# Optimization experiments

Hardware: AMD Instinct MI355X
Metric: run time of the kernel (lower is better)

Reference implementation:

```python
import jax, jax.numpy as jnp
import numpy as np

DT = 0.05
DELAY = int(1.0 / DT)  # 20 steps of synaptic delay
NUM_ASCS = 2
R_MEM = 0.1     # membrane resistance
SIGMA_V = 1.0   # sigmoid smoothing of spiking nonlinearity
V_RESET = 0.0

B, T, IN, HID, OUT = 64, 200, 512, 1024, 512


def setup_inputs() -> dict:
    key = jax.random.key(0)
    ks = jax.random.split(key, 10)
    return {
        "x": jax.random.normal(ks[0], (B, T, IN), dtype=jnp.float32),
        "W_in": jax.random.normal(ks[1], (IN, HID), dtype=jnp.float32) / np.sqrt(IN),
        "W_lat": jax.random.normal(ks[2], (HID, HID), dtype=jnp.float32) / np.sqrt(HID),
        "thresh": jax.random.normal(ks[3], (1, HID), dtype=jnp.float32) * 0.1,
        "trans_k_m": jax.random.normal(ks[4], (1, HID), dtype=jnp.float32) * 0.1,
        "trans_asc_k": jax.random.normal(ks[5], (NUM_ASCS, 1, HID), dtype=jnp.float32) * 0.1,
        "asc_amp": jax.random.normal(ks[6], (NUM_ASCS, 1, HID), dtype=jnp.float32) * 0.1,
        "trans_asc_r": jax.random.normal(ks[7], (NUM_ASCS, 1, HID), dtype=jnp.float32) * 0.1,
        "W_out": jax.random.normal(ks[8], (OUT, HID), dtype=jnp.float32) / np.sqrt(HID),
        "b_out": jax.random.normal(ks[9], (OUT,), dtype=jnp.float32) * 0.01,
    }


def _glifr_rnn(x, W_in, W_lat, thresh, trans_k_m, trans_asc_k, asc_amp, trans_asc_r, W_out, b_out):
    Bx, Tx, _ = x.shape
    H = W_lat.shape[0]
    # rate transforms keep dt*k in (0,1); r in (-1,1)
    k_m = jax.nn.sigmoid(trans_k_m) / DT          # [1,H]
    k_asc = jax.nn.sigmoid(trans_asc_k) / DT      # [A,1,H]
    asc_r = 1.0 - 2.0 * jax.nn.sigmoid(trans_asc_r)
    # precompute input projection for all timesteps: [T,B,H]
    x_proj = jnp.swapaxes(jnp.einsum("bti,ih->bth", x, W_in), 0, 1)

    def step(carry, xp):
        firing, voltage, asc, buf = carry
        firing_delayed = buf[0]                       # firing DELAY steps ago
        syn = xp + firing_delayed @ W_lat             # synaptic current [B,H]
        asc_new = (asc_amp + asc_r * asc) * firing * (DT * k_asc) + (1.0 - DT * k_asc) * asc
        volt_new = (R_MEM * DT * k_m) * (syn + asc_new.sum(0)) \
                   + (1.0 - DT * k_m) * voltage + DT * k_m * V_RESET
        firing_new = jax.nn.sigmoid((volt_new - thresh) / SIGMA_V)
        buf_new = jnp.concatenate([buf[1:], firing_new[None]], axis=0)
        out = firing_new @ W_out.T + b_out            # per-step linear readout
        return (firing_new, volt_new, asc_new, buf_new), out

    z = jnp.zeros((Bx, H), dtype=x.dtype)
    carry0 = (z, z, jnp.zeros((NUM_ASCS, Bx, H), x.dtype), jnp.zeros((DELAY, Bx, H), x.dtype))
    _, outs = jax.lax.scan(step, carry0, x_proj)      # outs: [T,B,OUT]
    return jnp.swapaxes(outs, 0, 1)                   # [B,T,OUT]


def reference(x, W_in, W_lat, thresh, trans_k_m, trans_asc_k, asc_amp, trans_asc_r, W_out, b_out):
    return _glifr_rnn(x, W_in, W_lat, thresh, trans_k_m, trans_asc_k, asc_amp, trans_asc_r, W_out, b_out)
```

## Files before the change

kernel.cpp:

```cpp
#include <hip/hip_runtime.h>


typedef float f32x4 __attribute__((ext_vector_type(4)));
typedef __bf16 bf16x8 __attribute__((ext_vector_type(8)));
typedef unsigned short ushortx8 __attribute__((ext_vector_type(8)));
typedef unsigned short ushortx4 __attribute__((ext_vector_type(4)));

__device__ __forceinline__ unsigned short f2b(float f) {
    unsigned int u = __float_as_uint(f);
    unsigned int r = u + 0x7FFFu + ((u >> 16) & 1u);
    return (unsigned short)(r >> 16);
}
__device__ __forceinline__ float b2f(unsigned short u) {
    return __uint_as_float(((unsigned int)u) << 16);
}
__device__ __forceinline__ float sigmoidf(float x) {
    return 1.0f / (1.0f + __expf(-x));
}

__device__ __forceinline__ void gl_lds16(const unsigned short* g, unsigned short* l) {
    __builtin_amdgcn_global_load_lds(
        (const __attribute__((address_space(1))) void*)g,
        (__attribute__((address_space(3))) void*)l, 16, 0, 0);
}

__global__ __launch_bounds__(256) void prep_all(
    const float* __restrict__ W_in, const float* __restrict__ W_lat,
    const float* __restrict__ W_out, const float* __restrict__ x,
    unsigned short* __restrict__ WinT, unsigned short* __restrict__ WlatT,
    unsigned short* __restrict__ WoutB, unsigned short* __restrict__ xb)
{
    __shared__ unsigned short t[64][65];
    const int blk = blockIdx.x, tid = threadIdx.x;

    if (blk < 128) {
        int bx = (blk & 15) * 64, by = (blk >> 4) * 64;
        int tx = tid & 63, ty = tid >> 6;
        for (int r = ty; r < 64; r += 4)
            t[r][tx] = f2b(W_in[(size_t)(by + r) * 1024 + bx + tx]);
        __syncthreads();
        for (int r = ty; r < 64; r += 4)
            WinT[(size_t)(bx + r) * 512 + by + tx] = t[tx][r];
    } else if (blk < 384) {
        int b2 = blk - 128;
        int bx = (b2 & 15) * 64, by = (b2 >> 4) * 64;
        int tx = tid & 63, ty = tid >> 6;
        for (int r = ty; r < 64; r += 4)
            t[r][tx] = f2b(W_lat[(size_t)(by + r) * 1024 + bx + tx]);
        __syncthreads();
        for (int r = ty; r < 64; r += 4)
            WlatT[(size_t)(bx + r) * 1024 + by + tx] = t[tx][r];
    } else if (blk < 896) {
        int i = ((blk - 384) * 256 + tid) * 4;
        f32x4 v = *(const f32x4*)(W_out + i);
        ushortx4 o;
        o[0] = f2b(v[0]); o[1] = f2b(v[1]); o[2] = f2b(v[2]); o[3] = f2b(v[3]);
        *(ushortx4*)(WoutB + i) = o;
    } else {
        size_t i8 = (size_t)((blk - 896) * 256 + tid) * 8;
        int m = (int)(i8 >> 9), k = (int)(i8 & 511);
        int b = m & 63, tt = m >> 6;
        const float* src = x + ((size_t)b * 200 + tt) * 512 + k;
        f32x4 v0 = *(const f32x4*)src;
        f32x4 v1 = *(const f32x4*)(src + 4);
        ushortx8 o;
        o[0] = f2b(v0[0]); o[1] = f2b(v0[1]); o[2] = f2b(v0[2]); o[3] = f2b(v0[3]);
        o[4] = f2b(v1[0]); o[5] = f2b(v1[1]); o[6] = f2b(v1[2]); o[7] = f2b(v1[3]);
        *(ushortx8*)(xb + i8) = o;
    }
}

template<int BM, int BN, int MODE>
__global__ __launch_bounds__(256) void gemm_nt(
    const unsigned short* __restrict__ A,
    const unsigned short* __restrict__ Bt,
    float* __restrict__ outf,
    unsigned short* __restrict__ outb,
    const float* __restrict__ bias,
    int M, int N, int K, int t_base)
{
    constexpr int WM = BM / 2, WN = BN / 2;
    constexpr int TM = WM / 16, TN = WN / 16;

    __shared__ unsigned short Asm[BM * 64];
    __shared__ unsigned short Bsm[BN * 64];

    const int tid  = threadIdx.x;
    const int wave = tid >> 6, lane = tid & 63;
    const int m16  = lane & 15, quad = lane >> 4;
    const int nwg = gridDim.x * gridDim.y;
    const int d   = blockIdx.y * gridDim.x + blockIdx.x;
    const int l   = (d & 7) * (nwg >> 3) + (d >> 3);
    const int bm0 = (l / gridDim.x) * BM, bn0 = (l % gridDim.x) * BN;
    const int wr   = (wave >> 1) * WM, wc = (wave & 1) * WN;
    const int sr   = lane >> 3;
    const int sc   = lane & 7;

    f32x4 acc[TM][TN];
#pragma unroll
    for (int i = 0; i < TM; i++)
#pragma unroll
        for (int j = 0; j < TN; j++)
            acc[i][j] = (f32x4){0.f, 0.f, 0.f, 0.f};

    for (int k0 = 0; k0 < K; k0 += 64) {
#pragma unroll
        for (int g = wave; g < BM / 8; g += 4) {
            int r = g * 8 + sr;
            int c = sc ^ (r & 7);
            gl_lds16(A + (size_t)(bm0 + r) * K + k0 + c * 8, Asm + g * 512);
        }
#pragma unroll
        for (int g = wave; g < BN / 8; g += 4) {
            int r = g * 8 + sr;
            int c = sc ^ (r & 7);
            gl_lds16(Bt + (size_t)(bn0 + r) * K + k0 + c * 8, Bsm + g * 512);
        }
        __syncthreads();

        ushortx8 af[2][TM], bfr[2][TN];
#pragma unroll
        for (int kh = 0; kh < 2; kh++) {
#pragma unroll
            for (int i = 0; i < TM; i++) {
                int ra = wr + i * 16 + m16;
                af[kh][i] = *(const ushortx8*)(
                    Asm + ra * 64 + (((kh * 4 + quad) ^ (ra & 7)) * 8));
            }
#pragma unroll
            for (int j = 0; j < TN; j++) {
                int rb = wc + j * 16 + m16;
                bfr[kh][j] = *(const ushortx8*)(
                    Bsm + rb * 64 + (((kh * 4 + quad) ^ (rb & 7)) * 8));
            }
        }
#pragma unroll
        for (int i = 0; i < TM; i++)
#pragma unroll
            for (int j = 0; j < TN; j++) {
                acc[i][j] = __builtin_amdgcn_mfma_f32_16x16x32_bf16(
                    __builtin_bit_cast(bf16x8, af[0][i]),
                    __builtin_bit_cast(bf16x8, bfr[0][j]),
                    acc[i][j], 0, 0, 0);
                acc[i][j] = __builtin_amdgcn_mfma_f32_16x16x32_bf16(
                    __builtin_bit_cast(bf16x8, af[1][i]),
                    __builtin_bit_cast(bf16x8, bfr[1][j]),
                    acc[i][j], 0, 0, 0);
            }
        __syncthreads();
    }

#pragma unroll
    for (int i = 0; i < TM; i++)
#pragma unroll
        for (int j = 0; j < TN; j++) {
            int col = bn0 + wc + j * 16 + m16;
            float bv = (MODE == 2) ? bias[col] : 0.f;
#pragma unroll
            for (int v = 0; v < 4; v++) {
                int row = bm0 + wr + i * 16 + quad * 4 + v;
                if (MODE == 2) {
                    size_t o = (size_t)((row & 63) * 200 + t_base + (row >> 6)) * N + col;
                    outf[o] = acc[i][j][v] + bv;
                } else {
                    outb[(size_t)row * N + col] = f2b(acc[i][j][v]);
                }
            }
        }
}

__global__ __launch_bounds__(256) void fused_chunk(
    const unsigned short* __restrict__ Fprev,
    const unsigned short* __restrict__ Wlat,
    const unsigned short* __restrict__ xproj,
    float* __restrict__ state,
    unsigned short* __restrict__ Fc,
    const float* __restrict__ thresh,
    const float* __restrict__ t_km,
    const float* __restrict__ t_ak,
    const float* __restrict__ amp,
    const float* __restrict__ t_ar,
    int first)
{
    const int BH = 64 * 1024;
    __shared__ __align__(16) char lds[147456];
    unsigned short* A0 = (unsigned short*)lds;
    unsigned short* A1 = (unsigned short*)(lds + 40960);
    unsigned short* B0 = (unsigned short*)(lds + 81920);
    unsigned short* B1 = (unsigned short*)(lds + 114688);
    float* synT = (float*)lds;

    const int tid  = threadIdx.x;
    const int wave = tid >> 6, lane = tid & 63;
    const int m16  = lane & 15, quad = lane >> 4;
    const int sr2  = lane >> 5;
    const int sc32 = lane & 31;
    const int d    = blockIdx.y * 16 + blockIdx.x;
    const int l    = (d & 7) * 32 + (d >> 3);
    const int b0   = (l >> 4) * 4, h0 = (l & 15) * 64;
    const int wrow = (wave >> 1) * 48;
    const int wc   = (wave & 1) * 32;

    const int h    = h0 + lane;
    const int gidx = (b0 + wave) * 1024 + h;
    float th  = thresh[h];
    float sm  = sigmoidf(t_km[h]);
    float rm  = 0.1f * sm;
    float om  = 1.0f - sm;
    float sa0 = sigmoidf(t_ak[h]);
    float sa1 = sigmoidf(t_ak[1024 + h]);
    float am0 = amp[h];
    float am1 = amp[1024 + h];
    float r0  = 1.0f - 2.0f * sigmoidf(t_ar[h]);
    float r1  = 1.0f - 2.0f * sigmoidf(t_ar[1024 + h]);

    if (first) {
        float volt = 0.f, as0 = 0.f, as1 = 0.f, fir = 0.f;
#pragma unroll
        for (int s = 0; s < 20; s++) {
            float sv  = b2f(xproj[(size_t)(s * 64 + b0 + wave) * 1024 + h]);
            float na0 = (am0 + r0 * as0) * fir * sa0 + (1.f - sa0) * as0;
            float na1 = (am1 + r1 * as1) * fir * sa1 + (1.f - sa1) * as1;
            volt = rm * (sv + na0 + na1) + om * volt;
            fir  = sigmoidf(volt - th);
            Fc[(size_t)s * BH + gidx] = f2b(fir);
            as0 = na0; as1 = na1;
        }
        state[gidx]          = volt;
        state[BH + gidx]     = as0;
        state[2 * BH + gidx] = as1;
        state[3 * BH + gidx] = fir;
        return;
    }

    f32x4 acc[3][2];
#pragma unroll
    for (int i = 0; i < 3; i++) {
        if (i < 2 || wave < 2) {
#pragma unroll
            for (int j = 0; j < 2; j++)
#pragma unroll
                for (int v = 0; v < 4; v++) {
                    int row = wrow + i * 16 + quad * 4 + v;
                    int col = h0 + wc + j * 16 + m16;
                    acc[i][j][v] = b2f(
                        xproj[(size_t)(((row >> 2) << 6) + b0 + (row & 3)) * 1024 + col]);
                }
        }
    }

    auto STAGE = [&](unsigned short* Ad, unsigned short* Bd, int k0) {
        for (int g = wave; g < 40; g += 4) {
            int r = g * 2 + sr2;
            int c = sc32 ^ (r & 31);
            int m = ((r >> 2) << 6) + b0 + (r & 3);
            gl_lds16(Fprev + (size_t)m * 1024 + k0 + c * 8, Ad + g * 512);
        }
        for (int g = wave; g < 32; g += 4) {
            int r = g * 2 + sr2;
            int c = sc32 ^ (r & 31);
            gl_lds16(Wlat + (size_t)(h0 + r) * 1024 + k0 + c * 8, Bd + g * 512);
        }
    };
    auto COMPUTE = [&](const unsigned short* As, const unsigned short* Bs) {
#pragma unroll
        for (int half = 0; half < 2; half++) {
            ushortx8 af[4][3], bfr[4][2];
#pragma unroll
            for (int kh = 0; kh < 4; kh++) {
                int s = half * 16 + kh * 4 + quad;
#pragma unroll
                for (int i = 0; i < 3; i++) {
                    if (i < 2 || wave < 2) {
                        int ra = wrow + i * 16 + m16;
                        af[kh][i] = *(const ushortx8*)(
                            As + ra * 256 + ((s ^ (ra & 31)) * 8));
                    }
                }
#pragma unroll
                for (int j = 0; j < 2; j++) {
                    int rb = wc + j * 16 + m16;
                    bfr[kh][j] = *(const ushortx8*)(
                        Bs + rb * 256 + ((s ^ (rb & 31)) * 8));
                }
            }
#pragma unroll
            for (int i = 0; i < 3; i++) {
                if (i < 2 || wave < 2) {
#pragma unroll
                    for (int j = 0; j < 2; j++) {
#pragma unroll
                        for (int kh = 0; kh < 4; kh++) {
                            acc[i][j] = __builtin_amdgcn_mfma_f32_16x16x32_bf16(
                                __builtin_bit_cast(bf16x8, af[kh][i]),
                                __builtin_bit_cast(bf16x8, bfr[kh][j]), acc[i][j], 0, 0, 0);
                        }
                    }
                }
            }
        }
    };

    STAGE(A0, B0, 0);
    __syncthreads();
    STAGE(A1, B1, 256);  COMPUTE(A0, B0);  __syncthreads();
    STAGE(A0, B0, 512);  COMPUTE(A1, B1);  __syncthreads();
    STAGE(A1, B1, 768);  COMPUTE(A0, B0);  __syncthreads();
                         COMPUTE(A1, B1);  __syncthreads();

#pragma unroll
    for (int i = 0; i < 3; i++) {
        if (i < 2 || wave < 2) {
#pragma unroll
            for (int j = 0; j < 2; j++)
#pragma unroll
                for (int v = 0; v < 4; v++) {
                    int row = wrow + i * 16 + quad * 4 + v;
                    synT[row * 66 + wc + j * 16 + m16] = acc[i][j][v];
                }
        }
    }
    __syncthreads();

    float volt = state[gidx];
    float as0  = state[BH + gidx];
    float as1  = state[2 * BH + gidx];
    float fir  = state[3 * BH + gidx];

#pragma unroll
    for (int s = 0; s < 20; s++) {
        float sv  = synT[(s * 4 + wave) * 66 + lane];
        float na0 = (am0 + r0 * as0) * fir * sa0 + (1.f - sa0) * as0;
        float na1 = (am1 + r1 * as1) * fir * sa1 + (1.f - sa1) * as1;
        volt = rm * (sv + na0 + na1) + om * volt;
        fir  = sigmoidf(volt - th);
        Fc[(size_t)s * BH + gidx] = f2b(fir);
        as0 = na0; as1 = na1;
    }
    state[gidx]          = volt;
    state[BH + gidx]     = as0;
    state[2 * BH + gidx] = as1;
    state[3 * BH + gidx] = fir;
}

extern "C" void kernel_launch(void* const* d_in, const int* in_sizes, int n_in,
                              void* d_out, int out_size, void* d_ws, size_t ws_size,
                              hipStream_t stream)
{
    const float* x      = (const float*)d_in[0];
    const float* W_in   = (const float*)d_in[1];
    const float* W_lat  = (const float*)d_in[2];
    const float* thresh = (const float*)d_in[3];
    const float* t_km   = (const float*)d_in[4];
    const float* t_ak   = (const float*)d_in[5];
    const float* amp    = (const float*)d_in[6];
    const float* t_ar   = (const float*)d_in[7];
    const float* W_out  = (const float*)d_in[8];
    const float* b_out  = (const float*)d_in[9];
    float* out = (float*)d_out;

    char* ws = (char*)d_ws;
    unsigned short* synb  = (unsigned short*)ws;
    float*          state = (float*)(ws + 52428800);
    unsigned short* F     = (unsigned short*)(ws + 53477376);
    unsigned short* xb    = F;
    unsigned short* WinT  = (unsigned short*)(ws + 79691776);
    unsigned short* WlatT = (unsigned short*)(ws + 80740352);
    unsigned short* WoutB = (unsigned short*)(ws + 82837504);

    prep_all<<<4096, 256, 0, stream>>>(W_in, W_lat, W_out, x,
                                       WinT, WlatT, WoutB, xb);

    gemm_nt<128, 128, 0><<<dim3(1024 / 128, 12800 / 128), 256, 0, stream>>>(
        xb, WinT, nullptr, synb, nullptr, 12800, 1024, 512, 0);

    const size_t CHUNK = 20 * 64 * 1024;
    fused_chunk<<<dim3(16, 16), 256, 0, stream>>>(
        F, WlatT, synb, state, F, thresh, t_km, t_ak, amp, t_ar, 1);
    for (int c = 1; c < 10; c++) {
        fused_chunk<<<dim3(16, 16), 256, 0, stream>>>(
            F + (size_t)(c - 1) * CHUNK, WlatT,
            synb + (size_t)c * CHUNK, state, F + (size_t)c * CHUNK,
            thresh, t_km, t_ak, amp, t_ar, 0);
    }

    gemm_nt<128, 128, 2><<<dim3(512 / 128, 12800 / 128), 256, 0, stream>>>(
        F, WoutB, out, nullptr, b_out, 12800, 512, 1024, 0);
}
```

Baseline: 242.5 us.

## Split fused chunk kernel over 512 blocks with smaller batch tiles and K-steps

Each fused_chunk block now covers 2 batch rows instead of 4, so the grid grows from 256 to 512 blocks to fill more compute units. The K loop is restaged in 128-wide steps with 16-way swizzle, which shrinks LDS from 144KB to 56KB and could let more than one block share a CU. Each wave now computes a 40x16 output tile with three MFMA row tiles, the last one partly wasted. Only 128 of 256 threads run the serial recurrence, and W_lat is re-read by twice as many blocks.

```diff
diff --git a/kernel.cpp b/kernel.cpp
--- a/kernel.cpp
+++ b/kernel.cpp
@@ -183,42 +183,153 @@
     int first)
 {
     const int BH = 64 * 1024;
-    __shared__ __align__(16) char lds[147456];
+    __shared__ __align__(16) char lds[57344];
     unsigned short* A0 = (unsigned short*)lds;
-    unsigned short* A1 = (unsigned short*)(lds + 40960);
-    unsigned short* B0 = (unsigned short*)(lds + 81920);
-    unsigned short* B1 = (unsigned short*)(lds + 114688);
+    unsigned short* A1 = (unsigned short*)(lds + 12288);
+    unsigned short* B0 = (unsigned short*)(lds + 24576);
+    unsigned short* B1 = (unsigned short*)(lds + 40960);
     float* synT = (float*)lds;
 
     const int tid  = threadIdx.x;
     const int wave = tid >> 6, lane = tid & 63;
     const int m16  = lane & 15, quad = lane >> 4;
-    const int sr2  = lane >> 5;
-    const int sc32 = lane & 31;
+    const int sr4  = lane >> 4;
+    const int sc16 = lane & 15;
     const int d    = blockIdx.y * 16 + blockIdx.x;
-    const int l    = (d & 7) * 32 + (d >> 3);
-    const int b0   = (l >> 4) * 4, h0 = (l & 15) * 64;
-    const int wrow = (wave >> 1) * 48;
-    const int wc   = (wave & 1) * 32;
-
-    const int h    = h0 + lane;
-    const int gidx = (b0 + wave) * 1024 + h;
-    float th  = thresh[h];
-    float sm  = sigmoidf(t_km[h]);
-    float rm  = 0.1f * sm;
-    float om  = 1.0f - sm;
-    float sa0 = sigmoidf(t_ak[h]);
-    float sa1 = sigmoidf(t_ak[1024 + h]);
-    float am0 = amp[h];
-    float am1 = amp[1024 + h];
-    float r0  = 1.0f - 2.0f * sigmoidf(t_ar[h]);
-    float r1  = 1.0f - 2.0f * sigmoidf(t_ar[1024 + h]);
+    const int l    = (d & 7) * 64 + (d >> 3);
+    const int bg   = l >> 4;
+    const int h0   = (l & 15) * 64, b0 = bg * 2;
+    const int wc   = wave * 16;
 
     if (first) {
-        float volt = 0.f, as0 = 0.f, as1 = 0.f, fir = 0.f;
+        if (tid < 128) {
+            const int b_local = tid >> 6, h_local = tid & 63;
+            const int h    = h0 + h_local;
+            const int gidx = (b0 + b_local) * 1024 + h;
+            float th  = thresh[h];
+            float sm  = sigmoidf(t_km[h]);
+            float rm  = 0.1f * sm;
+            float om  = 1.0f - sm;
+            float sa0 = sigmoidf(t_ak[h]);
+            float sa1 = sigmoidf(t_ak[1024 + h]);
+            float am0 = amp[h];
+            float am1 = amp[1024 + h];
+            float r0  = 1.0f - 2.0f * sigmoidf(t_ar[h]);
+            float r1  = 1.0f - 2.0f * sigmoidf(t_ar[1024 + h]);
+            float volt = 0.f, as0 = 0.f, as1 = 0.f, fir = 0.f;
+#pragma unroll
+            for (int s = 0; s < 20; s++) {
+                float sv  = b2f(xproj[(size_t)(s * 64 + b0 + b_local) * 1024 + h]);
+                float na0 = (am0 + r0 * as0) * fir * sa0 + (1.f - sa0) * as0;
+                float na1 = (am1 + r1 * as1) * fir * sa1 + (1.f - sa1) * as1;
+                volt = rm * (sv + na0 + na1) + om * volt;
+                fir  = sigmoidf(volt - th);
+                Fc[(size_t)s * BH + gidx] = f2b(fir);
+                as0 = na0; as1 = na1;
+            }
+            state[gidx]          = volt;
+            state[BH + gidx]     = as0;
+            state[2 * BH + gidx] = as1;
+            state[3 * BH + gidx] = fir;
+        }
+        return;
+    }
+
+    f32x4 acc[3];
+#pragma unroll
+    for (int i = 0; i < 3; i++) {
+#pragma unroll
+        for (int v = 0; v < 4; v++) {
+            int row = i * 16 + quad * 4 + v;
+            int col = h0 + wc + m16;
+            acc[i][v] = (row < 40)
+                ? b2f(xproj[(size_t)(((row >> 1) << 6) + b0 + (row & 1)) * 1024 + col])
+                : 0.f;
+        }
+    }
+
+    auto STAGE = [&](unsigned short* Ad, unsigned short* Bd, int k0) {
+        for (int g = wave; g < 10; g += 4) {
+            int r = g * 4 + sr4;
+            int c = sc16 ^ (r & 15);
+            int m = ((r >> 1) << 6) + b0 + (r & 1);
+            gl_lds16(Fprev + (size_t)m * 1024 + k0 + c * 8, Ad + g * 512);
+        }
+        for (int g = wave; g < 16; g += 4) {
+            int r = g * 4 + sr4;
+            int c = sc16 ^ (r & 15);
+            gl_lds16(Wlat + (size_t)(h0 + r) * 1024 + k0 + c * 8, Bd + g * 512);
+        }
+    };
+    auto COMPUTE = [&](const unsigned short* As, const unsigned short* Bs) {
+        ushortx8 af[4][3], bfr[4];
+#pragma unroll
+        for (int kh = 0; kh < 4; kh++) {
+            int s = kh * 4 + quad;
+#pragma unroll
+            for (int i = 0; i < 3; i++) {
+                int ra = i * 16 + m16;
+                af[kh][i] = *(const ushortx8*)(
+                    As + ra * 128 + ((s ^ (ra & 15)) * 8));
+            }
+            int rb = wc + m16;
+            bfr[kh] = *(const ushortx8*)(
+                Bs + rb * 128 + ((s ^ (rb & 15)) * 8));
+        }
+#pragma unroll
+        for (int i = 0; i < 3; i++)
+#pragma unroll
+            for (int kh = 0; kh < 4; kh++)
+                acc[i] = __builtin_amdgcn_mfma_f32_16x16x32_bf16(
+                    __builtin_bit_cast(bf16x8, af[kh][i]),
+                    __builtin_bit_cast(bf16x8, bfr[kh]), acc[i], 0, 0, 0);
+    };
+
+    STAGE(A0, B0, 0);
+    __syncthreads();
+    STAGE(A1, B1, 128);  COMPUTE(A0, B0);  __syncthreads();
+    STAGE(A0, B0, 256);  COMPUTE(A1, B1);  __syncthreads();
+    STAGE(A1, B1, 384);  COMPUTE(A0, B0);  __syncthreads();
+    STAGE(A0, B0, 512);  COMPUTE(A1, B1);  __syncthreads();
+    STAGE(A1, B1, 640);  COMPUTE(A0, B0);  __syncthreads();
+    STAGE(A0, B0, 768);  COMPUTE(A1, B1);  __syncthreads();
+    STAGE(A1, B1, 896);  COMPUTE(A0, B0);  __syncthreads();
+                         COMPUTE(A1, B1);  __syncthreads();
+
+#pragma unroll
+    for (int i = 0; i < 3; i++) {
+#pragma unroll
+        for (int v = 0; v < 4; v++) {
+            int row = i * 16 + quad * 4 + v;
+            if (row < 40)
+                synT[row * 66 + wc + m16] = acc[i][v];
+        }
+    }
+    __syncthreads();
+
+    if (tid < 128) {
+        const int b_local = tid >> 6, h_local = tid & 63;
+        const int h    = h0 + h_local;
+        const int gidx = (b0 + b_local) * 1024 + h;
+        float th  = thresh[h];
+        float sm  = sigmoidf(t_km[h]);
+        float rm  = 0.1f * sm;
+        float om  = 1.0f - sm;
+        float sa0 = sigmoidf(t_ak[h]);
+        float sa1 = sigmoidf(t_ak[1024 + h]);
+        float am0 = amp[h];
+        float am1 = amp[1024 + h];
+        float r0  = 1.0f - 2.0f * sigmoidf(t_ar[h]);
+        float r1  = 1.0f - 2.0f * sigmoidf(t_ar[1024 + h]);
+
+        float volt = state[gidx];
+        float as0  = state[BH + gidx];
+        float as1  = state[2 * BH + gidx];
+        float fir  = state[3 * BH + gidx];
+
 #pragma unroll
         for (int s = 0; s < 20; s++) {
-            float sv  = b2f(xproj[(size_t)(s * 64 + b0 + wave) * 1024 + h]);
+            float sv  = synT[(s * 2 + b_local) * 66 + h_local];
             float na0 = (am0 + r0 * as0) * fir * sa0 + (1.f - sa0) * as0;
             float na1 = (am1 + r1 * as1) * fir * sa1 + (1.f - sa1) * as1;
             volt = rm * (sv + na0 + na1) + om * volt;
@@ -230,117 +341,7 @@
         state[BH + gidx]     = as0;
         state[2 * BH + gidx] = as1;
         state[3 * BH + gidx] = fir;
-        return;
-    }
-
-    f32x4 acc[3][2];
-#pragma unroll
-    for (int i = 0; i < 3; i++) {
-        if (i < 2 || wave < 2) {
-#pragma unroll
-            for (int j = 0; j < 2; j++)
-#pragma unroll
-                for (int v = 0; v < 4; v++) {
-                    int row = wrow + i * 16 + quad * 4 + v;
-                    int col = h0 + wc + j * 16 + m16;
-                    acc[i][j][v] = b2f(
-                        xproj[(size_t)(((row >> 2) << 6) + b0 + (row & 3)) * 1024 + col]);
-                }
-        }
-    }
-
-    auto STAGE = [&](unsigned short* Ad, unsigned short* Bd, int k0) {
-        for (int g = wave; g < 40; g += 4) {
-            int r = g * 2 + sr2;
-            int c = sc32 ^ (r & 31);
-            int m = ((r >> 2) << 6) + b0 + (r & 3);
-            gl_lds16(Fprev + (size_t)m * 1024 + k0 + c * 8, Ad + g * 512);
-        }
-        for (int g = wave; g < 32; g += 4) {
-            int r = g * 2 + sr2;
-            int c = sc32 ^ (r & 31);
-            gl_lds16(Wlat + (size_t)(h0 + r) * 1024 + k0 + c * 8, Bd + g * 512);
-        }
-    };
-    auto COMPUTE = [&](const unsigned short* As, const unsigned short* Bs) {
-#pragma unroll
-        for (int half = 0; half < 2; half++) {
-            ushortx8 af[4][3], bfr[4][2];
-#pragma unroll
-            for (int kh = 0; kh < 4; kh++) {
-                int s = half * 16 + kh * 4 + quad;
-#pragma unroll
-                for (int i = 0; i < 3; i++) {
-                    if (i < 2 || wave < 2) {
-                        int ra = wrow + i * 16 + m16;
-                        af[kh][i] = *(const ushortx8*)(
-                            As + ra * 256 + ((s ^ (ra & 31)) * 8));
-                    }
-                }
-#pragma unroll
-                for (int j = 0; j < 2; j++) {
-                    int rb = wc + j * 16 + m16;
-                    bfr[kh][j] = *(const ushortx8*)(
-                        Bs + rb * 256 + ((s ^ (rb & 31)) * 8));
-                }
-            }
-#pragma unroll
-            for (int i = 0; i < 3; i++) {
-                if (i < 2 || wave < 2) {
-#pragma unroll
-                    for (int j = 0; j < 2; j++) {
-#pragma unroll
-                        for (int kh = 0; kh < 4; kh++) {
-                            acc[i][j] = __builtin_amdgcn_mfma_f32_16x16x32_bf16(
-                                __builtin_bit_cast(bf16x8, af[kh][i]),
-                                __builtin_bit_cast(bf16x8, bfr[kh][j]), acc[i][j], 0, 0, 0);
-                        }
-                    }
-                }
-            }
-        }
-    };
-
-    STAGE(A0, B0, 0);
-    __syncthreads();
-    STAGE(A1, B1, 256);  COMPUTE(A0, B0);  __syncthreads();
-    STAGE(A0, B0, 512);  COMPUTE(A1, B1);  __syncthreads();
-    STAGE(A1, B1, 768);  COMPUTE(A0, B0);  __syncthreads();
-                         COMPUTE(A1, B1);  __syncthreads();
-
-#pragma unroll
-    for (int i = 0; i < 3; i++) {
-        if (i < 2 || wave < 2) {
-#pragma unroll
-            for (int j = 0; j < 2; j++)
-#pragma unroll
-                for (int v = 0; v < 4; v++) {
-                    int row = wrow + i * 16 + quad * 4 + v;
-                    synT[row * 66 + wc + j * 16 + m16] = acc[i][j][v];
-                }
-        }
-    }
-    __syncthreads();
-
-    float volt = state[gidx];
-    float as0  = state[BH + gidx];
-    float as1  = state[2 * BH + gidx];
-    float fir  = state[3 * BH + gidx];
-
-#pragma unroll
-    for (int s = 0; s < 20; s++) {
-        float sv  = synT[(s * 4 + wave) * 66 + lane];
-        float na0 = (am0 + r0 * as0) * fir * sa0 + (1.f - sa0) * as0;
-        float na1 = (am1 + r1 * as1) * fir * sa1 + (1.f - sa1) * as1;
-        volt = rm * (sv + na0 + na1) + om * volt;
-        fir  = sigmoidf(volt - th);
-        Fc[(size_t)s * BH + gidx] = f2b(fir);
-        as0 = na0; as1 = na1;
-    }
-    state[gidx]          = volt;
-    state[BH + gidx]     = as0;
-    state[2 * BH + gidx] = as1;
-    state[3 * BH + gidx] = fir;
+    }
 }
 
 extern "C" void kernel_launch(void* const* d_in, const int* in_sizes, int n_in,
@@ -375,10 +376,10 @@
         xb, WinT, nullptr, synb, nullptr, 12800, 1024, 512, 0);
 
     const size_t CHUNK = 20 * 64 * 1024;
-    fused_chunk<<<dim3(16, 16), 256, 0, stream>>>(
+    fused_chunk<<<dim3(16, 32), 256, 0, stream>>>(
         F, WlatT, synb, state, F, thresh, t_km, t_ak, amp, t_ar, 1);
     for (int c = 1; c < 10; c++) {
-        fused_chunk<<<dim3(16, 16), 256, 0, stream>>>(
+        fused_chunk<<<dim3(16, 32), 256, 0, stream>>>(
             F + (size_t)(c - 1) * CHUNK, WlatT,
             synb + (size_t)c * CHUNK, state, F + (size_t)c * CHUNK,
             thresh, t_km, t_ak, amp, t_ar, 0);
```

New measurement: 259.8 us. 1.07x slower.

## Triple-buffer LDS staging with smaller K tiles and partial vmcnt waits

Applied to the files above, without the earlier changes.

Halves the K tile from 256 to 128 and switches from double to triple buffering, so the LDS footprint shrinks from 144KB to 108KB. Barriers now wait only until the oldest stage's global-to-LDS loads have landed (vmcnt(9)), which keeps two stages of loads in flight while computing. The aim is to hide global load latency in each chunk step. It adds more barrier rounds and relies on the hand-counted vmcnt matching the number of loads each wave issues per stage.

```diff
diff --git a/kernel.cpp b/kernel.cpp
--- a/kernel.cpp
+++ b/kernel.cpp
@@ -183,18 +183,20 @@
     int first)
 {
     const int BH = 64 * 1024;
-    __shared__ __align__(16) char lds[147456];
-    unsigned short* A0 = (unsigned short*)lds;
-    unsigned short* A1 = (unsigned short*)(lds + 40960);
-    unsigned short* B0 = (unsigned short*)(lds + 81920);
-    unsigned short* B1 = (unsigned short*)(lds + 114688);
+    __shared__ __align__(16) char lds[110592];
+    unsigned short* AX = (unsigned short*)lds;
+    unsigned short* BX = (unsigned short*)(lds + 20480);
+    unsigned short* AY = (unsigned short*)(lds + 36864);
+    unsigned short* BY = (unsigned short*)(lds + 57344);
+    unsigned short* AZ = (unsigned short*)(lds + 73728);
+    unsigned short* BZ = (unsigned short*)(lds + 94208);
     float* synT = (float*)lds;
 
     const int tid  = threadIdx.x;
     const int wave = tid >> 6, lane = tid & 63;
     const int m16  = lane & 15, quad = lane >> 4;
-    const int sr2  = lane >> 5;
-    const int sc32 = lane & 31;
+    const int sr4  = lane >> 4;
+    const int sc16 = lane & 15;
     const int d    = blockIdx.y * 16 + blockIdx.x;
     const int l    = (d & 7) * 32 + (d >> 3);
     const int b0   = (l >> 4) * 4, h0 = (l & 15) * 64;
@@ -250,63 +252,74 @@
     }
 
     auto STAGE = [&](unsigned short* Ad, unsigned short* Bd, int k0) {
-        for (int g = wave; g < 40; g += 4) {
-            int r = g * 2 + sr2;
-            int c = sc32 ^ (r & 31);
+        for (int g = wave; g < 20; g += 4) {
+            int r = g * 4 + sr4;
+            int c = sc16 ^ (r & 15);
             int m = ((r >> 2) << 6) + b0 + (r & 3);
             gl_lds16(Fprev + (size_t)m * 1024 + k0 + c * 8, Ad + g * 512);
         }
-        for (int g = wave; g < 32; g += 4) {
-            int r = g * 2 + sr2;
-            int c = sc32 ^ (r & 31);
+        for (int g = wave; g < 16; g += 4) {
+            int r = g * 4 + sr4;
+            int c = sc16 ^ (r & 15);
             gl_lds16(Wlat + (size_t)(h0 + r) * 1024 + k0 + c * 8, Bd + g * 512);
         }
     };
     auto COMPUTE = [&](const unsigned short* As, const unsigned short* Bs) {
-#pragma unroll
-        for (int half = 0; half < 2; half++) {
-            ushortx8 af[4][3], bfr[4][2];
-#pragma unroll
-            for (int kh = 0; kh < 4; kh++) {
-                int s = half * 16 + kh * 4 + quad;
-#pragma unroll
-                for (int i = 0; i < 3; i++) {
-                    if (i < 2 || wave < 2) {
-                        int ra = wrow + i * 16 + m16;
-                        af[kh][i] = *(const ushortx8*)(
-                            As + ra * 256 + ((s ^ (ra & 31)) * 8));
+        ushortx8 af[4][3], bfr[4][2];
+#pragma unroll
+        for (int kh = 0; kh < 4; kh++) {
+            int s = kh * 4 + quad;
+#pragma unroll
+            for (int i = 0; i < 3; i++) {
+                if (i < 2 || wave < 2) {
+                    int ra = wrow + i * 16 + m16;
+                    af[kh][i] = *(const ushortx8*)(
+                        As + ra * 128 + ((s ^ (ra & 15)) * 8));
+                }
+            }
+#pragma unroll
+            for (int j = 0; j < 2; j++) {
+                int rb = wc + j * 16 + m16;
+                bfr[kh][j] = *(const ushortx8*)(
+                    Bs + rb * 128 + ((s ^ (rb & 15)) * 8));
+            }
+        }
+#pragma unroll
+        for (int i = 0; i < 3; i++) {
+            if (i < 2 || wave < 2) {
+#pragma unroll
+                for (int j = 0; j < 2; j++) {
+#pragma unroll
+                    for (int kh = 0; kh < 4; kh++) {
+                        acc[i][j] = __builtin_amdgcn_mfma_f32_16x16x32_bf16(
+                            __builtin_bit_cast(bf16x8, af[kh][i]),
+                            __builtin_bit_cast(bf16x8, bfr[kh][j]), acc[i][j], 0, 0, 0);
                     }
                 }
-#pragma unroll
-                for (int j = 0; j < 2; j++) {
-                    int rb = wc + j * 16 + m16;
-                    bfr[kh][j] = *(const ushortx8*)(
-                        Bs + rb * 256 + ((s ^ (rb & 31)) * 8));
-                }
-            }
-#pragma unroll
-            for (int i = 0; i < 3; i++) {
-                if (i < 2 || wave < 2) {
-#pragma unroll
-                    for (int j = 0; j < 2; j++) {
-#pragma unroll
-                        for (int kh = 0; kh < 4; kh++) {
-                            acc[i][j] = __builtin_amdgcn_mfma_f32_16x16x32_bf16(
-                                __builtin_bit_cast(bf16x8, af[kh][i]),
-                                __builtin_bit_cast(bf16x8, bfr[kh][j]), acc[i][j], 0, 0, 0);
-                        }
-                    }
-                }
             }
         }
     };
 
-    STAGE(A0, B0, 0);
+#define W9B() do { asm volatile("s_waitcnt vmcnt(9) lgkmcnt(0)" ::: "memory"); \
+                   __builtin_amdgcn_s_barrier(); } while (0)
+#define W0B() do { asm volatile("s_waitcnt vmcnt(0) lgkmcnt(0)" ::: "memory"); \
+                   __builtin_amdgcn_s_barrier(); } while (0)
+
+    STAGE(AX, BX, 0);
+    STAGE(AY, BY, 128);
+    W9B();
+    STAGE(AZ, BZ, 256);  COMPUTE(AX, BX);  W9B();
+    STAGE(AX, BX, 384);  COMPUTE(AY, BY);  W9B();
+    STAGE(AY, BY, 512);  COMPUTE(AZ, BZ);  W9B();
+    STAGE(AZ, BZ, 640);  COMPUTE(AX, BX);  W9B();
+    STAGE(AX, BX, 768);  COMPUTE(AY, BY);  W9B();
+    STAGE(AY, BY, 896);  COMPUTE(AZ, BZ);  W9B();
+                         COMPUTE(AX, BX);  W0B();
+                         COMPUTE(AY, BY);
     __syncthreads();
-    STAGE(A1, B1, 256);  COMPUTE(A0, B0);  __syncthreads();
-    STAGE(A0, B0, 512);  COMPUTE(A1, B1);  __syncthreads();
-    STAGE(A1, B1, 768);  COMPUTE(A0, B0);  __syncthreads();
-                         COMPUTE(A1, B1);  __syncthreads();
+
+#undef W9B
+#undef W0B
 
 #pragma unroll
     for (int i = 0; i < 3; i++) {
```

After: 245.6 us. About the same (+1.3%).
